# Performance work log

Hardware: AMD Instinct MI355X
Metric: run time of the kernel (lower is better)

The kernel has to match this reference:

```python
import jax, jax.numpy as jnp
import numpy as np

# Winograd F(4x4, 3x3) transform matrices (m=4, r=3, a=6)
B_T = jnp.array([[4.,0.,-5.,0.,1.,0.],
                 [0.,-4.,-4.,1.,1.,0.],
                 [0.,4.,-4.,-1.,1.,0.],
                 [0.,-2.,-1.,2.,1.,0.],
                 [0.,2.,-1.,-2.,1.,0.],
                 [0.,4.,0.,-5.,0.,1.]], dtype=jnp.float32)
G = jnp.array([[1/4.,0.,0.],
               [-1/6.,-1/6.,-1/6.],
               [-1/6.,1/6.,-1/6.],
               [1/24.,1/12.,1/6.],
               [1/24.,-1/12.,1/6.],
               [0.,0.,1.]], dtype=jnp.float32)
A_T = jnp.array([[1.,1.,1.,1.,1.,0.],
                 [0.,1.,-1.,2.,-2.,0.],
                 [0.,1.,1.,4.,4.,0.],
                 [0.,1.,-1.,8.,-8.,1.]], dtype=jnp.float32)

M_OUT, R_K, A_IN = 4, 3, 6  # output tile m, kernel r, input tile a = m+r-1


def setup_inputs() -> dict:
    key = jax.random.key(0)
    k1, k2 = jax.random.split(key)
    x = jax.random.normal(k1, (16, 64, 130, 130), dtype=jnp.float32)
    w = jax.random.normal(k2, (64, 64, 3, 3), dtype=jnp.float32) * 0.05
    return {"input": x, "weight": w}


def reference(input, weight):
    N, C, H, W = input.shape
    K = weight.shape[0]
    m, r, a = M_OUT, R_K, A_IN
    T = (H - r + 1) // m  # tiles per spatial dim (perfect tiling)

    # Filter transform: U[k,c] = G @ w[k,c] @ G^T  -> [K,C,a,a]
    U = jnp.einsum('ai,kcij,bj->kcab', G, weight, G)

    # Extract overlapping a x a input tiles with stride m: [N,C,T,a,T,a]
    idx = (jnp.arange(T) * m)[:, None] + jnp.arange(a)[None, :]  # [T,a]
    tiles = input[:, :, idx, :][:, :, :, :, idx]

    # Input transform: V = B^T @ tile @ B  -> [N,T,T,C,a,a]
    V = jnp.einsum('ai,nctisj,bj->ntscab', B_T, tiles, B_T)
    Vp = V.reshape(N * T * T, C, a, a)  # [P,C,a,a]

    # Elementwise (tile-domain) multiply + channel reduce: M[p,k] = sum_c U[k,c]*V[p,c]
    Mt = jnp.einsum('kcab,pcab->pkab', U, Vp)  # [P,K,a,a]

    # Output transform: Y_tile = A^T @ M @ A -> [P,K,m,m]
    Yt = jnp.einsum('ai,pkij,bj->pkab', A_T, Mt, A_T)

    out = T * m  # = H - r + 1
    Y = Yt.reshape(N, T, T, K, m, m).transpose(0, 3, 1, 4, 2, 5).reshape(N, K, out, out)
    return Y
```

## Files before the change

kernel.cpp:

```cpp
#include <hip/hip_runtime.h>


__constant__ float c_AT[24] = {
  1.f, 0.f, 0.f, 0.f,
  1.f, 1.f, 1.f, 1.f,
  1.f,-1.f, 1.f,-1.f,
  1.f, 2.f, 4.f, 8.f,
  1.f,-2.f, 4.f,-8.f,
  0.f, 0.f, 0.f, 1.f
};

__device__ __forceinline__ void gl2lds16(const float* g, float* l) {
  __builtin_amdgcn_global_load_lds((const __attribute__((address_space(1))) void*)g,
                                   (__attribute__((address_space(3))) void*)l, 16, 0, 0);
}

__global__ __launch_bounds__(256) void k_filter(const float* __restrict__ w,
                                                float* __restrict__ U) {
  int g = blockIdx.x * 256 + threadIdx.x;
  int k = g & 63;
  int c = g >> 6;
  const float* wp = w + (size_t)(k * 64 + c) * 9;
  float w00 = wp[0], w01 = wp[1], w02 = wp[2];
  float w10 = wp[3], w11 = wp[4], w12 = wp[5];
  float w20 = wp[6], w21 = wp[7], w22 = wp[8];
  const float G[6][3] = {
    {0.25f, 0.f, 0.f},
    {-1.f/6.f, -1.f/6.f, -1.f/6.f},
    {-1.f/6.f,  1.f/6.f, -1.f/6.f},
    {1.f/24.f,  1.f/12.f, 1.f/6.f},
    {1.f/24.f, -1.f/12.f, 1.f/6.f},
    {0.f, 0.f, 1.f}
  };
  float t[6][3];
#pragma unroll
  for (int a = 0; a < 6; ++a) {
    t[a][0] = G[a][0]*w00 + G[a][1]*w10 + G[a][2]*w20;
    t[a][1] = G[a][0]*w01 + G[a][1]*w11 + G[a][2]*w21;
    t[a][2] = G[a][0]*w02 + G[a][1]*w12 + G[a][2]*w22;
  }
#pragma unroll
  for (int a = 0; a < 6; ++a) {
#pragma unroll
    for (int b = 0; b < 6; ++b) {
      float u = G[b][0]*t[a][0] + G[b][1]*t[a][1] + G[b][2]*t[a][2];
      U[(size_t)(a*6+b)*4096 + c*64 + k] = u;
    }
  }
}

__global__ __launch_bounds__(256) void k_input(const float* __restrict__ x,
                                               float* __restrict__ V,
                                               int n0, int Pchunk) {
  __shared__ float Ls[34*134];
  const int tid  = threadIdx.x;
  const int bi   = blockIdx.x;
  const int band = bi & 3;
  const int c    = (bi >> 2) & 63;
  const int nl   = bi >> 8;
  const float* xp = x + (size_t)((n0 + nl) * 64 + c) * (130*130) + band * 32 * 130;
  for (int idx = tid; idx < 34*65; idx += 256) {
    int r  = idx / 65;
    int c2 = idx - r * 65;
    *(float2*)&Ls[r*134 + c2*2] = *(const float2*)(xp + r*130 + c2*2);
  }
  __syncthreads();
  const int tyl = tid >> 5;
  const int tx  = tid & 31;
  const int ty  = band * 8 + tyl;
  const int p   = (nl * 32 + ty) * 32 + tx;
  const float* bl = &Ls[(tyl*4)*134 + tx*4];
  float t1[6][6];
#pragma unroll
  for (int j = 0; j < 6; ++j) {
    float d0 = bl[0*134+j], d1 = bl[1*134+j], d2 = bl[2*134+j];
    float d3 = bl[3*134+j], d4 = bl[4*134+j], d5 = bl[5*134+j];
    t1[0][j] =  4.f*d0 - 5.f*d2 + d4;
    t1[1][j] = -4.f*d1 - 4.f*d2 + d3 + d4;
    t1[2][j] =  4.f*d1 - 4.f*d2 - d3 + d4;
    t1[3][j] = -2.f*d1 -     d2 + 2.f*d3 + d4;
    t1[4][j] =  2.f*d1 -     d2 - 2.f*d3 + d4;
    t1[5][j] =  4.f*d1 - 5.f*d3 + d5;
  }
  float* vb = V + (size_t)c * Pchunk + p;
  const size_t abs_ = (size_t)64 * Pchunk;
#pragma unroll
  for (int a = 0; a < 6; ++a) {
    float s0=t1[a][0], s1=t1[a][1], s2=t1[a][2], s3=t1[a][3], s4=t1[a][4], s5=t1[a][5];
    float v0 =  4.f*s0 - 5.f*s2 + s4;
    float v1 = -4.f*s1 - 4.f*s2 + s3 + s4;
    float v2 =  4.f*s1 - 4.f*s2 - s3 + s4;
    float v3 = -2.f*s1 -     s2 + 2.f*s3 + s4;
    float v4 =  2.f*s1 -     s2 - 2.f*s3 + s4;
    float v5 =  4.f*s1 - 5.f*s3 + s5;
    vb[(size_t)(a*6+0)*abs_] = v0;
    vb[(size_t)(a*6+1)*abs_] = v1;
    vb[(size_t)(a*6+2)*abs_] = v2;
    vb[(size_t)(a*6+3)*abs_] = v3;
    vb[(size_t)(a*6+4)*abs_] = v4;
    vb[(size_t)(a*6+5)*abs_] = v5;
  }
}

__global__ __launch_bounds__(256) void k_gemm2(const float* __restrict__ V,
                                               const float* __restrict__ U,
                                               float* __restrict__ M,
                                               int Pchunk, int nPB) {
  __shared__ float Vs[64*256];
  __shared__ float Us[64*64];
  const int tid  = threadIdx.x;
  const int lane = tid & 63;
  const int wv   = tid >> 6;
  const unsigned bx = blockIdx.x;
  const int ab = bx / (unsigned)nPB;
  const int pb = bx - ab * nPB;
  const int p0 = pb * 256;

  const float* Vab = V + (size_t)ab * 64 * Pchunk + p0;
  const float* Uab = U + (size_t)ab * 4096;

#pragma unroll
  for (int i = 0; i < 16; ++i) {
    int r = wv + i * 4;
    gl2lds16(Vab + (size_t)r * Pchunk + lane * 4, &Vs[r * 256]);
  }
#pragma unroll
  for (int i = 0; i < 4; ++i) {
    int li = wv + i * 4;
    gl2lds16(Uab + li * 256 + lane * 4, &Us[li * 256]);
  }
  __syncthreads();

  const int pt = tid & 31;
  const int kt = tid >> 5;
  float acc[8][8];
#pragma unroll
  for (int ki = 0; ki < 8; ++ki)
#pragma unroll
    for (int pi = 0; pi < 8; ++pi) acc[ki][pi] = 0.f;

#pragma unroll 4
  for (int c = 0; c < 64; ++c) {
    const float4 va = *(const float4*)&Vs[c*256 + pt*4];
    const float4 vb = *(const float4*)&Vs[c*256 + 128 + pt*4];
    const float4 ua = *(const float4*)&Us[c*64 + kt*8];
    const float4 ub = *(const float4*)&Us[c*64 + kt*8 + 4];
    const float vv[8] = {va.x, va.y, va.z, va.w, vb.x, vb.y, vb.z, vb.w};
    const float uu[8] = {ua.x, ua.y, ua.z, ua.w, ub.x, ub.y, ub.z, ub.w};
#pragma unroll
    for (int ki = 0; ki < 8; ++ki)
#pragma unroll
      for (int pi = 0; pi < 8; ++pi)
        acc[ki][pi] += uu[ki] * vv[pi];
  }

#pragma unroll
  for (int ki = 0; ki < 8; ++ki) {
    float* mb = M + ((size_t)ab * 64 + kt*8 + ki) * Pchunk + p0;
    *(float4*)(mb + pt*4)       = make_float4(acc[ki][0], acc[ki][1], acc[ki][2], acc[ki][3]);
    *(float4*)(mb + 128 + pt*4) = make_float4(acc[ki][4], acc[ki][5], acc[ki][6], acc[ki][7]);
  }
}

__global__ __launch_bounds__(256) void k_out(const float* __restrict__ M,
                                             float* __restrict__ out,
                                             int n0, int Pchunk, int bpk) {
  const unsigned bx = blockIdx.x;
  const int k    = bx / (unsigned)bpk;
  const int pblk = bx - k * bpk;
  const int p    = pblk * 256 + threadIdx.x;
  const int nl = p >> 10;
  const int ty = (p >> 5) & 31;
  const int tx = p & 31;

  const float* mp = M + (size_t)k * Pchunk + p;
  const size_t abstride = (size_t)64 * Pchunk;
  float m[36];
#pragma unroll
  for (int ab = 0; ab < 36; ++ab) m[ab] = mp[(size_t)ab * abstride];

  float Y[4][4];
#pragma unroll
  for (int u = 0; u < 4; ++u)
#pragma unroll
    for (int v = 0; v < 4; ++v) Y[u][v] = 0.f;

#pragma unroll
  for (int i = 0; i < 6; ++i) {
    float R[4] = {0.f, 0.f, 0.f, 0.f};
#pragma unroll
    for (int j = 0; j < 6; ++j) {
      float mm = m[i*6 + j];
#pragma unroll
      for (int v = 0; v < 4; ++v) R[v] += c_AT[j*4 + v] * mm;
    }
#pragma unroll
    for (int u = 0; u < 4; ++u) {
      float au = c_AT[i*4 + u];
#pragma unroll
      for (int v = 0; v < 4; ++v) Y[u][v] += au * R[v];
    }
  }

  float* ob = out + ((size_t)((n0 + nl) * 64 + k) * 128 + ty*4) * 128 + tx*4;
#pragma unroll
  for (int u = 0; u < 4; ++u)
    *(float4*)(ob + (size_t)u * 128) = make_float4(Y[u][0], Y[u][1], Y[u][2], Y[u][3]);
}

extern "C" void kernel_launch(void* const* d_in, const int* in_sizes, int n_in,
                              void* d_out, int out_size, void* d_ws, size_t ws_size,
                              hipStream_t stream) {
  const float* x = (const float*)d_in[0];
  const float* w = (const float*)d_in[1];
  float* out = (float*)d_out;
  float* U = (float*)d_ws;
  const size_t U_bytes = 36ull * 64 * 64 * 4;
  const size_t per_n = 2ull * 36 * 1024 * 64 * 4;
  size_t avail = ws_size > U_bytes ? ws_size - U_bytes : 0;
  int chunk = (int)(avail / per_n);
  if (chunk < 1) return;
  if (chunk > 16) chunk = 16;

  k_filter<<<16, 256, 0, stream>>>(w, U);
  for (int n0 = 0; n0 < 16; n0 += chunk) {
    int cn = (16 - n0) < chunk ? (16 - n0) : chunk;
    int Pchunk = cn * 1024;
    float* V = (float*)((char*)d_ws + U_bytes);
    float* M = V + (size_t)36 * 64 * Pchunk;
    int nPB = cn * 4;
    k_input<<<cn*256,  256, 0, stream>>>(x, V, n0, Pchunk);
    k_gemm2<<<36*nPB,  256, 0, stream>>>(V, U, M, Pchunk, nPB);
    k_out  <<<64*nPB,  256, 0, stream>>>(M, out, n0, Pchunk, nPB);
  }
}
```

Measured before the change: 268.3 us.

## Use split-bf16 MFMA GEMM fused with output transform, drop M buffer

Replaces the fp32 FMA batched GEMM and separate output-transform kernel with a single fused kernel. It splits U and V into bf16 hi/lo pairs and accumulates three MFMA 16x16x32 products per tile, with double-buffered LDS staging. It applies the A^T output transform in registers, so the intermediate M tensor never goes to memory. The input transform is reorganised into a channel-contiguous bf16 layout, and the N-chunking loop is removed. The bf16x3 split drops the lo*lo term, which costs some precision, and the strided 2-byte scattered stores in k_input2 may be inefficient.

```diff
diff --git a/kernel.cpp b/kernel.cpp
--- a/kernel.cpp
+++ b/kernel.cpp
@@ -1,22 +1,21 @@
 #include <hip/hip_runtime.h>
 
 
-__constant__ float c_AT[24] = {
-  1.f, 0.f, 0.f, 0.f,
-  1.f, 1.f, 1.f, 1.f,
-  1.f,-1.f, 1.f,-1.f,
-  1.f, 2.f, 4.f, 8.f,
-  1.f,-2.f, 4.f,-8.f,
-  0.f, 0.f, 0.f, 1.f
-};
-
-__device__ __forceinline__ void gl2lds16(const float* g, float* l) {
-  __builtin_amdgcn_global_load_lds((const __attribute__((address_space(1))) void*)g,
-                                   (__attribute__((address_space(3))) void*)l, 16, 0, 0);
+typedef __attribute__((ext_vector_type(8))) short bf16x8;
+typedef __attribute__((ext_vector_type(4))) float f32x4;
+
+__device__ __forceinline__ unsigned short f2bf(float x) {
+  unsigned u = __float_as_uint(x);
+  u = u + 0x7fffu + ((u >> 16) & 1u);
+  return (unsigned short)(u >> 16);
+}
+__device__ __forceinline__ float bf2f(unsigned short h) {
+  return __uint_as_float(((unsigned)h) << 16);
 }
 
 __global__ __launch_bounds__(256) void k_filter(const float* __restrict__ w,
-                                                float* __restrict__ U) {
+                                                unsigned short* __restrict__ Uhi,
+                                                unsigned short* __restrict__ Ulo) {
   int g = blockIdx.x * 256 + threadIdx.x;
   int k = g & 63;
   int c = g >> 6;
@@ -44,168 +43,190 @@
 #pragma unroll
     for (int b = 0; b < 6; ++b) {
       float u = G[b][0]*t[a][0] + G[b][1]*t[a][1] + G[b][2]*t[a][2];
-      U[(size_t)(a*6+b)*4096 + c*64 + k] = u;
-    }
-  }
-}
-
-__global__ __launch_bounds__(256) void k_input(const float* __restrict__ x,
-                                               float* __restrict__ V,
-                                               int n0, int Pchunk) {
-  __shared__ float Ls[34*134];
-  const int tid  = threadIdx.x;
-  const int bi   = blockIdx.x;
-  const int band = bi & 3;
-  const int c    = (bi >> 2) & 63;
-  const int nl   = bi >> 8;
-  const float* xp = x + (size_t)((n0 + nl) * 64 + c) * (130*130) + band * 32 * 130;
-  for (int idx = tid; idx < 34*65; idx += 256) {
-    int r  = idx / 65;
-    int c2 = idx - r * 65;
-    *(float2*)&Ls[r*134 + c2*2] = *(const float2*)(xp + r*130 + c2*2);
-  }
-  __syncthreads();
-  const int tyl = tid >> 5;
-  const int tx  = tid & 31;
-  const int ty  = band * 8 + tyl;
-  const int p   = (nl * 32 + ty) * 32 + tx;
-  const float* bl = &Ls[(tyl*4)*134 + tx*4];
-  float t1[6][6];
-#pragma unroll
-  for (int j = 0; j < 6; ++j) {
-    float d0 = bl[0*134+j], d1 = bl[1*134+j], d2 = bl[2*134+j];
-    float d3 = bl[3*134+j], d4 = bl[4*134+j], d5 = bl[5*134+j];
-    t1[0][j] =  4.f*d0 - 5.f*d2 + d4;
-    t1[1][j] = -4.f*d1 - 4.f*d2 + d3 + d4;
-    t1[2][j] =  4.f*d1 - 4.f*d2 - d3 + d4;
-    t1[3][j] = -2.f*d1 -     d2 + 2.f*d3 + d4;
-    t1[4][j] =  2.f*d1 -     d2 - 2.f*d3 + d4;
-    t1[5][j] =  4.f*d1 - 5.f*d3 + d5;
-  }
-  float* vb = V + (size_t)c * Pchunk + p;
-  const size_t abs_ = (size_t)64 * Pchunk;
-#pragma unroll
-  for (int a = 0; a < 6; ++a) {
-    float s0=t1[a][0], s1=t1[a][1], s2=t1[a][2], s3=t1[a][3], s4=t1[a][4], s5=t1[a][5];
-    float v0 =  4.f*s0 - 5.f*s2 + s4;
-    float v1 = -4.f*s1 - 4.f*s2 + s3 + s4;
-    float v2 =  4.f*s1 - 4.f*s2 - s3 + s4;
-    float v3 = -2.f*s1 -     s2 + 2.f*s3 + s4;
-    float v4 =  2.f*s1 -     s2 - 2.f*s3 + s4;
-    float v5 =  4.f*s1 - 5.f*s3 + s5;
-    vb[(size_t)(a*6+0)*abs_] = v0;
-    vb[(size_t)(a*6+1)*abs_] = v1;
-    vb[(size_t)(a*6+2)*abs_] = v2;
-    vb[(size_t)(a*6+3)*abs_] = v3;
-    vb[(size_t)(a*6+4)*abs_] = v4;
-    vb[(size_t)(a*6+5)*abs_] = v5;
-  }
-}
-
-__global__ __launch_bounds__(256) void k_gemm2(const float* __restrict__ V,
-                                               const float* __restrict__ U,
-                                               float* __restrict__ M,
-                                               int Pchunk, int nPB) {
-  __shared__ float Vs[64*256];
-  __shared__ float Us[64*64];
+      unsigned short hi = f2bf(u);
+      unsigned short lo = f2bf(u - bf2f(hi));
+      size_t e = ((size_t)(a*6 + b) * 64 + k) * 64 + c;
+      Uhi[e] = hi; Ulo[e] = lo;
+    }
+  }
+}
+
+__global__ __launch_bounds__(256) void k_input2(const float* __restrict__ x,
+                                                unsigned short* __restrict__ Vhi,
+                                                unsigned short* __restrict__ Vlo) {
+  __shared__ float Ls[16*6*132];
+  const int tid = threadIdx.x;
+  const int nl  = blockIdx.x >> 5;
+  const int ty  = blockIdx.x & 31;
+  const int cl  = tid & 15;
+  const int tx0 = tid >> 4;
+
+  for (int cg = 0; cg < 4; ++cg) {
+    if (cg) __syncthreads();
+    for (int idx = tid; idx < 16*6*65; idx += 256) {
+      int c16 = idx / 390;
+      int rem = idx - c16 * 390;
+      int r   = rem / 65;
+      int c2  = rem - r * 65;
+      const float* src = x + ((size_t)((nl*64 + cg*16 + c16) * 130 + (ty*4 + r))) * 130 + c2*2;
+      *(float2*)&Ls[(c16*6 + r)*132 + c2*2] = *(const float2*)src;
+    }
+    __syncthreads();
+    const int cc = cg*16 + cl;
+#pragma unroll
+    for (int h = 0; h < 2; ++h) {
+      const int tx = tx0 + h*16;
+      const int p  = (nl*32 + ty)*32 + tx;
+      const float* bl = &Ls[(cl*6)*132 + tx*4];
+      float t1[6][6];
+#pragma unroll
+      for (int j = 0; j < 6; ++j) {
+        float d0 = bl[0*132+j], d1 = bl[1*132+j], d2 = bl[2*132+j];
+        float d3 = bl[3*132+j], d4 = bl[4*132+j], d5 = bl[5*132+j];
+        t1[0][j] =  4.f*d0 - 5.f*d2 + d4;
+        t1[1][j] = -4.f*d1 - 4.f*d2 + d3 + d4;
+        t1[2][j] =  4.f*d1 - 4.f*d2 - d3 + d4;
+        t1[3][j] = -2.f*d1 -     d2 + 2.f*d3 + d4;
+        t1[4][j] =  2.f*d1 -     d2 - 2.f*d3 + d4;
+        t1[5][j] =  4.f*d1 - 5.f*d3 + d5;
+      }
+#pragma unroll
+      for (int a = 0; a < 6; ++a) {
+        float s0=t1[a][0], s1=t1[a][1], s2=t1[a][2], s3=t1[a][3], s4=t1[a][4], s5=t1[a][5];
+        float vv[6];
+        vv[0] =  4.f*s0 - 5.f*s2 + s4;
+        vv[1] = -4.f*s1 - 4.f*s2 + s3 + s4;
+        vv[2] =  4.f*s1 - 4.f*s2 - s3 + s4;
+        vv[3] = -2.f*s1 -     s2 + 2.f*s3 + s4;
+        vv[4] =  2.f*s1 -     s2 - 2.f*s3 + s4;
+        vv[5] =  4.f*s1 - 5.f*s3 + s5;
+#pragma unroll
+        for (int b = 0; b < 6; ++b) {
+          unsigned short hi = f2bf(vv[b]);
+          unsigned short lo = f2bf(vv[b] - bf2f(hi));
+          size_t e = ((size_t)(a*6 + b) * 16384 + p) * 64 + cc;
+          Vhi[e] = hi; Vlo[e] = lo;
+        }
+      }
+    }
+  }
+}
+
+__global__ __launch_bounds__(256) void k_fused(const unsigned short* __restrict__ Uhi,
+                                               const unsigned short* __restrict__ Ulo,
+                                               const unsigned short* __restrict__ Vhi,
+                                               const unsigned short* __restrict__ Vlo,
+                                               float* __restrict__ out) {
+  __shared__ __align__(16) float LdsF[2*23040/4];
+  char* Lds = (char*)LdsF;
   const int tid  = threadIdx.x;
   const int lane = tid & 63;
   const int wv   = tid >> 6;
-  const unsigned bx = blockIdx.x;
-  const int ab = bx / (unsigned)nPB;
-  const int pb = bx - ab * nPB;
-  const int p0 = pb * 256;
-
-  const float* Vab = V + (size_t)ab * 64 * Pchunk + p0;
-  const float* Uab = U + (size_t)ab * 4096;
-
-#pragma unroll
-  for (int i = 0; i < 16; ++i) {
-    int r = wv + i * 4;
-    gl2lds16(Vab + (size_t)r * Pchunk + lane * 4, &Vs[r * 256]);
-  }
-#pragma unroll
-  for (int i = 0; i < 4; ++i) {
-    int li = wv + i * 4;
-    gl2lds16(Uab + li * 256 + lane * 4, &Us[li * 256]);
+  const int p0   = blockIdx.x * 16;
+
+  const char* gb[5]; size_t gst[5]; int lo_[5];
+  {
+    int q0 = tid, q1 = tid + 256;
+    gb[0] = (const char*)Uhi + q0*16; gst[0] = 8192; lo_[0] =        (q0>>3)*144 + (q0&7)*16;
+    gb[1] = (const char*)Uhi + q1*16; gst[1] = 8192; lo_[1] =        (q1>>3)*144 + (q1&7)*16;
+    gb[2] = (const char*)Ulo + q0*16; gst[2] = 8192; lo_[2] = 9216 + (q0>>3)*144 + (q0&7)*16;
+    gb[3] = (const char*)Ulo + q1*16; gst[3] = 8192; lo_[3] = 9216 + (q1>>3)*144 + (q1&7)*16;
+    if (tid < 128) {
+      int q = tid;
+      gb[4] = (const char*)Vhi + (size_t)(p0 + (q>>3))*128 + (q&7)*16;
+      gst[4] = (size_t)16384*128; lo_[4] = 18432 + (q>>3)*144 + (q&7)*16;
+    } else {
+      int q = tid - 128;
+      gb[4] = (const char*)Vlo + (size_t)(p0 + (q>>3))*128 + (q&7)*16;
+      gst[4] = (size_t)16384*128; lo_[4] = 20736 + (q>>3)*144 + (q&7)*16;
+    }
+  }
+
+  float Yv[4][16];
+#pragma unroll
+  for (int r = 0; r < 4; ++r)
+#pragma unroll
+    for (int q = 0; q < 16; ++q) Yv[r][q] = 0.f;
+
+  const float AT4[4][6] = {
+    {1.f, 1.f,  1.f, 1.f,  1.f, 0.f},
+    {0.f, 1.f, -1.f, 2.f, -2.f, 0.f},
+    {0.f, 1.f,  1.f, 4.f,  4.f, 0.f},
+    {0.f, 1.f, -1.f, 8.f, -8.f, 1.f}
+  };
+
+  {
+    float4 s0[5];
+#pragma unroll
+    for (int i = 0; i < 5; ++i) s0[i] = *(const float4*)(gb[i]);
+#pragma unroll
+    for (int i = 0; i < 5; ++i) *(float4*)(Lds + lo_[i]) = s0[i];
   }
   __syncthreads();
 
-  const int pt = tid & 31;
-  const int kt = tid >> 5;
-  float acc[8][8];
-#pragma unroll
-  for (int ki = 0; ki < 8; ++ki)
-#pragma unroll
-    for (int pi = 0; pi < 8; ++pi) acc[ki][pi] = 0.f;
-
-#pragma unroll 4
-  for (int c = 0; c < 64; ++c) {
-    const float4 va = *(const float4*)&Vs[c*256 + pt*4];
-    const float4 vb = *(const float4*)&Vs[c*256 + 128 + pt*4];
-    const float4 ua = *(const float4*)&Us[c*64 + kt*8];
-    const float4 ub = *(const float4*)&Us[c*64 + kt*8 + 4];
-    const float vv[8] = {va.x, va.y, va.z, va.w, vb.x, vb.y, vb.z, vb.w};
-    const float uu[8] = {ua.x, ua.y, ua.z, ua.w, ub.x, ub.y, ub.z, ub.w};
-#pragma unroll
-    for (int ki = 0; ki < 8; ++ki)
-#pragma unroll
-      for (int pi = 0; pi < 8; ++pi)
-        acc[ki][pi] += uu[ki] * vv[pi];
-  }
-
-#pragma unroll
-  for (int ki = 0; ki < 8; ++ki) {
-    float* mb = M + ((size_t)ab * 64 + kt*8 + ki) * Pchunk + p0;
-    *(float4*)(mb + pt*4)       = make_float4(acc[ki][0], acc[ki][1], acc[ki][2], acc[ki][3]);
-    *(float4*)(mb + 128 + pt*4) = make_float4(acc[ki][4], acc[ki][5], acc[ki][6], acc[ki][7]);
-  }
-}
-
-__global__ __launch_bounds__(256) void k_out(const float* __restrict__ M,
-                                             float* __restrict__ out,
-                                             int n0, int Pchunk, int bpk) {
-  const unsigned bx = blockIdx.x;
-  const int k    = bx / (unsigned)bpk;
-  const int pblk = bx - k * bpk;
-  const int p    = pblk * 256 + threadIdx.x;
-  const int nl = p >> 10;
+  int bsel = 0;
+#pragma unroll
+  for (int a6 = 0; a6 < 6; ++a6) {
+#pragma unroll
+    for (int b6 = 0; b6 < 6; ++b6) {
+      const int ab = a6*6 + b6;
+      float4 sreg[5];
+      if (ab < 35) {
+#pragma unroll
+        for (int i = 0; i < 5; ++i)
+          sreg[i] = *(const float4*)(gb[i] + (size_t)(ab + 1) * gst[i]);
+      }
+      const char* B0 = Lds + bsel*23040;
+      f32x4 m4 = {0.f, 0.f, 0.f, 0.f};
+      const int arow = wv*16 + (lane & 15);
+      const int brow = (lane & 15);
+#pragma unroll
+      for (int s = 0; s < 2; ++s) {
+        const int g = (lane >> 4) + 4*s;
+        bf16x8 ah  = *(const bf16x8*)(B0 +         arow*144 + g*16);
+        bf16x8 al  = *(const bf16x8*)(B0 +  9216 + arow*144 + g*16);
+        bf16x8 bh  = *(const bf16x8*)(B0 + 18432 + brow*144 + g*16);
+        bf16x8 bl2 = *(const bf16x8*)(B0 + 20736 + brow*144 + g*16);
+        m4 = __builtin_amdgcn_mfma_f32_16x16x32_bf16(ah, bh,  m4, 0, 0, 0);
+        m4 = __builtin_amdgcn_mfma_f32_16x16x32_bf16(ah, bl2, m4, 0, 0, 0);
+        m4 = __builtin_amdgcn_mfma_f32_16x16x32_bf16(al, bh,  m4, 0, 0, 0);
+      }
+#pragma unroll
+      for (int u = 0; u < 4; ++u) {
+        const float cu = AT4[u][a6];
+        if (cu == 0.f) continue;
+#pragma unroll
+        for (int v = 0; v < 4; ++v) {
+          const float cv = AT4[v][b6];
+          if (cv == 0.f) continue;
+          const float cf = cu * cv;
+#pragma unroll
+          for (int r = 0; r < 4; ++r) Yv[r][u*4 + v] += cf * m4[r];
+        }
+      }
+      if (ab < 35) {
+        char* W0 = Lds + (bsel^1)*23040;
+#pragma unroll
+        for (int i = 0; i < 5; ++i) *(float4*)(W0 + lo_[i]) = sreg[i];
+      }
+      __syncthreads();
+      bsel ^= 1;
+    }
+  }
+
+  const int p  = p0 + (lane & 15);
+  const int n  = p >> 10;
   const int ty = (p >> 5) & 31;
   const int tx = p & 31;
-
-  const float* mp = M + (size_t)k * Pchunk + p;
-  const size_t abstride = (size_t)64 * Pchunk;
-  float m[36];
-#pragma unroll
-  for (int ab = 0; ab < 36; ++ab) m[ab] = mp[(size_t)ab * abstride];
-
-  float Y[4][4];
-#pragma unroll
-  for (int u = 0; u < 4; ++u)
-#pragma unroll
-    for (int v = 0; v < 4; ++v) Y[u][v] = 0.f;
-
-#pragma unroll
-  for (int i = 0; i < 6; ++i) {
-    float R[4] = {0.f, 0.f, 0.f, 0.f};
-#pragma unroll
-    for (int j = 0; j < 6; ++j) {
-      float mm = m[i*6 + j];
-#pragma unroll
-      for (int v = 0; v < 4; ++v) R[v] += c_AT[j*4 + v] * mm;
-    }
-#pragma unroll
-    for (int u = 0; u < 4; ++u) {
-      float au = c_AT[i*4 + u];
-#pragma unroll
-      for (int v = 0; v < 4; ++v) Y[u][v] += au * R[v];
-    }
-  }
-
-  float* ob = out + ((size_t)((n0 + nl) * 64 + k) * 128 + ty*4) * 128 + tx*4;
-#pragma unroll
-  for (int u = 0; u < 4; ++u)
-    *(float4*)(ob + (size_t)u * 128) = make_float4(Y[u][0], Y[u][1], Y[u][2], Y[u][3]);
+#pragma unroll
+  for (int r = 0; r < 4; ++r) {
+    const int k = wv*16 + (lane >> 4)*4 + r;
+    float* ob = out + ((size_t)(n*64 + k)*128 + ty*4)*128 + tx*4;
+#pragma unroll
+    for (int u = 0; u < 4; ++u)
+      *(float4*)(ob + (size_t)u*128) =
+        make_float4(Yv[r][u*4+0], Yv[r][u*4+1], Yv[r][u*4+2], Yv[r][u*4+3]);
+  }
 }
 
 extern "C" void kernel_launch(void* const* d_in, const int* in_sizes, int n_in,
@@ -214,23 +235,16 @@
   const float* x = (const float*)d_in[0];
   const float* w = (const float*)d_in[1];
   float* out = (float*)d_out;
-  float* U = (float*)d_ws;
-  const size_t U_bytes = 36ull * 64 * 64 * 4;
-  const size_t per_n = 2ull * 36 * 1024 * 64 * 4;
-  size_t avail = ws_size > U_bytes ? ws_size - U_bytes : 0;
-  int chunk = (int)(avail / per_n);
-  if (chunk < 1) return;
-  if (chunk > 16) chunk = 16;
-
-  k_filter<<<16, 256, 0, stream>>>(w, U);
-  for (int n0 = 0; n0 < 16; n0 += chunk) {
-    int cn = (16 - n0) < chunk ? (16 - n0) : chunk;
-    int Pchunk = cn * 1024;
-    float* V = (float*)((char*)d_ws + U_bytes);
-    float* M = V + (size_t)36 * 64 * Pchunk;
-    int nPB = cn * 4;
-    k_input<<<cn*256,  256, 0, stream>>>(x, V, n0, Pchunk);
-    k_gemm2<<<36*nPB,  256, 0, stream>>>(V, U, M, Pchunk, nPB);
-    k_out  <<<64*nPB,  256, 0, stream>>>(M, out, n0, Pchunk, nPB);
-  }
-}
+
+  unsigned short* Uhi = (unsigned short*)d_ws;
+  unsigned short* Ulo = Uhi + (size_t)36*64*64;
+  unsigned short* Vhi = Ulo + (size_t)36*64*64;
+  unsigned short* Vlo = Vhi + (size_t)36*16384*64;
+
+  const size_t need = (2ull*36*64*64 + 2ull*36*16384*64) * 2;
+  if (ws_size < need) return;
+
+  k_filter<<<16,   256, 0, stream>>>(w, Uhi, Ulo);
+  k_input2<<<512,  256, 0, stream>>>(x, Vhi, Vlo);
+  k_fused <<<1024, 256, 0, stream>>>(Uhi, Ulo, Vhi, Vlo, out);
+}
```

Measured after the change: 599.5 us. 123% more time.
